# Performance work log

Hardware: AMD Instinct MI355X
Metric: run time of the kernel (lower is better)

Reference implementation:

```python
import jax, jax.numpy as jnp
import numpy as np

B, IN, H = 4096, 1024, 1024


def setup_inputs() -> dict:
    key = jax.random.key(0)
    ks = jax.random.split(key, 16)
    s_in = 1.0 / np.sqrt(IN)
    s_h = 1.0 / np.sqrt(H)
    d = {
        "x_t": jax.random.normal(ks[0], (B, IN), jnp.float32),
        "h_prev": jax.random.normal(ks[1], (B, H), jnp.float32),
        "c_prev": jax.random.normal(ks[2], (B, H), jnp.float32),
    }
    # input->hidden weights (with bias), stored torch-style as (out, in)
    for i, name in enumerate(["ii", "if", "ig", "io"]):
        d[f"W_{name}"] = jax.random.uniform(ks[3 + i], (H, IN), jnp.float32, -s_in, s_in)
        d[f"b_{name}"] = jax.random.uniform(ks[7 + i], (H,), jnp.float32, -s_in, s_in)
    # hidden->hidden weights (no bias)
    for i, name in enumerate(["hi", "hf", "hg", "ho"]):
        d[f"W_{name}"] = jax.random.uniform(ks[11 + i], (H, H), jnp.float32, -s_h, s_h)
    return d


def reference(x_t, h_prev, c_prev,
              W_ii, b_ii, W_if, b_if, W_ig, b_ig, W_io, b_io,
              W_hi, W_hf, W_hg, W_ho):
    # Fuse the 8 small GEMMs into 2 concatenated GEMMs (same math).
    Wx = jnp.concatenate([W_ii, W_if, W_ig, W_io], axis=0)   # (4H, IN)
    Wh = jnp.concatenate([W_hi, W_hf, W_hg, W_ho], axis=0)   # (4H, H)
    b = jnp.concatenate([b_ii, b_if, b_ig, b_io], axis=0)    # (4H,)
    gates = x_t @ Wx.T + h_prev @ Wh.T + b                    # (B, 4H)
    zi, zf, zg, zo = jnp.split(gates, 4, axis=1)
    i_t = jax.nn.sigmoid(zi)
    f_t = jax.nn.sigmoid(zf)
    g_t = jnp.tanh(zg)
    o_t = jax.nn.sigmoid(zo)
    c_t = f_t * c_prev + i_t * g_t
    h_t = o_t * jnp.tanh(c_t)
    return (h_t, c_t, (i_t, f_t, g_t, o_t))
```

## Files before the change

kernel.cpp:

```cpp
#include <hip/hip_runtime.h>
#include <hip/hip_bf16.h>

#define B_DIM 4096
#define K_TOT 2048
#define N_TOT 4096
#define H_DIM 1024

typedef short bf16x8 __attribute__((ext_vector_type(8)));
typedef float f32x4 __attribute__((ext_vector_type(4)));
typedef unsigned short u16x8 __attribute__((ext_vector_type(8)));

typedef __attribute__((address_space(1))) const unsigned gas_u32;
typedef __attribute__((address_space(3))) unsigned las_u32;

static __device__ __forceinline__ unsigned short f2bf(float f) {
  union { float f; unsigned u; } v; v.f = f;
  unsigned r = v.u + 0x7FFF + ((v.u >> 16) & 1);
  return (unsigned short)(r >> 16);
}

__global__ void pack_a(const float* __restrict__ x, const float* __restrict__ hp,
                       u16x8* __restrict__ A) {
  int t = blockIdx.x * blockDim.x + threadIdx.x;
  int idx = t << 3;
  int b = idx >> 11;
  int k = idx & 2047;
  const float* src = (k < 1024) ? (x + b * 1024 + k) : (hp + b * 1024 + (k - 1024));
  float4 lo = *(const float4*)src;
  float4 hi = *(const float4*)(src + 4);
  u16x8 v;
  v[0] = f2bf(lo.x); v[1] = f2bf(lo.y); v[2] = f2bf(lo.z); v[3] = f2bf(lo.w);
  v[4] = f2bf(hi.x); v[5] = f2bf(hi.y); v[6] = f2bf(hi.z); v[7] = f2bf(hi.w);
  A[t] = v;
}

__global__ void pack_w(const float* __restrict__ W0, const float* __restrict__ W1,
                       const float* __restrict__ W2, const float* __restrict__ W3,
                       const float* __restrict__ W4, const float* __restrict__ W5,
                       const float* __restrict__ W6, const float* __restrict__ W7,
                       u16x8* __restrict__ Wc) {
  int t = blockIdx.x * blockDim.x + threadIdx.x;
  int idx = t << 3;
  int n = idx >> 11;
  int k = idx & 2047;
  int gate = n >> 10;
  int j = n & 1023;
  int s = (k < 1024) ? gate : gate + 4;
  const float* base =
      (s == 0) ? W0 : (s == 1) ? W1 : (s == 2) ? W2 : (s == 3) ? W3 :
      (s == 4) ? W4 : (s == 5) ? W5 : (s == 6) ? W6 : W7;
  const float* src = base + j * 1024 + (k & 1023);
  float4 lo = *(const float4*)src;
  float4 hi = *(const float4*)(src + 4);
  u16x8 v;
  v[0] = f2bf(lo.x); v[1] = f2bf(lo.y); v[2] = f2bf(lo.z); v[3] = f2bf(lo.w);
  v[4] = f2bf(hi.x); v[5] = f2bf(hi.y); v[6] = f2bf(hi.z); v[7] = f2bf(hi.w);
  Wc[t] = v;
}

__global__ __launch_bounds__(256) void gemm_gates(
    const unsigned short* __restrict__ A,
    const unsigned short* __restrict__ W,
    float* __restrict__ G) {
  __shared__ unsigned short As[128 * 32];
  __shared__ unsigned short Bs[128 * 32];
  const int tid = threadIdx.x;
  const int wave = tid >> 6;
  const int lane = tid & 63;
  const int m0 = blockIdx.y << 7;
  const int n0 = blockIdx.x << 7;
  const int wm = (wave >> 1) << 6;
  const int wn = (wave & 1) << 6;

  f32x4 acc[4][4];
#pragma unroll
  for (int mi = 0; mi < 4; ++mi)
#pragma unroll
    for (int ni = 0; ni < 4; ++ni)
      acc[mi][ni] = (f32x4){0.f, 0.f, 0.f, 0.f};

  const int c0 = wave * 2;
  const int srow = c0 * 16 + (lane >> 2);
  const int scol = (lane & 3) * 8;
  const unsigned short* aptr0 = A + (long)(m0 + srow) * K_TOT + scol;
  const unsigned short* aptr1 = A + (long)(m0 + srow + 16) * K_TOT + scol;
  const unsigned short* bptr0 = W + (long)(n0 + srow) * K_TOT + scol;
  const unsigned short* bptr1 = W + (long)(n0 + srow + 16) * K_TOT + scol;
  char* lA0 = (char*)As + c0 * 1024;
  char* lA1 = lA0 + 1024;
  char* lB0 = (char*)Bs + c0 * 1024;
  char* lB1 = lB0 + 1024;

  const int fr = lane & 15;
  const int fko = (lane >> 4) * 16;

  for (int k0 = 0; k0 < K_TOT; k0 += 32) {
    __builtin_amdgcn_global_load_lds((gas_u32*)(aptr0 + k0), (las_u32*)lA0, 16, 0, 0);
    __builtin_amdgcn_global_load_lds((gas_u32*)(aptr1 + k0), (las_u32*)lA1, 16, 0, 0);
    __builtin_amdgcn_global_load_lds((gas_u32*)(bptr0 + k0), (las_u32*)lB0, 16, 0, 0);
    __builtin_amdgcn_global_load_lds((gas_u32*)(bptr1 + k0), (las_u32*)lB1, 16, 0, 0);
    __syncthreads();
    bf16x8 af[4], bfv[4];
#pragma unroll
    for (int i = 0; i < 4; ++i) {
      af[i]  = *(const bf16x8*)((const char*)As + (wm + i * 16 + fr) * 64 + fko);
      bfv[i] = *(const bf16x8*)((const char*)Bs + (wn + i * 16 + fr) * 64 + fko);
    }
#pragma unroll
    for (int mi = 0; mi < 4; ++mi)
#pragma unroll
      for (int ni = 0; ni < 4; ++ni)
        acc[mi][ni] = __builtin_amdgcn_mfma_f32_16x16x32_bf16(af[mi], bfv[ni], acc[mi][ni], 0, 0, 0);
    __syncthreads();
  }

  const int ccol = lane & 15;
  const int crow = (lane >> 4) * 4;
#pragma unroll
  for (int mi = 0; mi < 4; ++mi) {
#pragma unroll
    for (int ni = 0; ni < 4; ++ni) {
      float* gp = G + (long)(m0 + wm + mi * 16 + crow) * N_TOT + (n0 + wn + ni * 16 + ccol);
      gp[0]                 = acc[mi][ni][0];
      gp[N_TOT]             = acc[mi][ni][1];
      gp[2 * (long)N_TOT]   = acc[mi][ni][2];
      gp[3 * (long)N_TOT]   = acc[mi][ni][3];
    }
  }
}

static __device__ __forceinline__ float sigm(float x) {
  return 1.0f / (1.0f + __expf(-x));
}
static __device__ __forceinline__ float tanh_fast(float x) {
  x = fminf(fmaxf(x, -15.f), 15.f);
  float t = __expf(-2.0f * x);
  return (1.0f - t) / (1.0f + t);
}

__global__ void lstm_pointwise(const float* __restrict__ G, const float* __restrict__ cp,
                               const float* __restrict__ bii, const float* __restrict__ bif,
                               const float* __restrict__ big, const float* __restrict__ bio,
                               float* __restrict__ out) {
  int t = blockIdx.x * blockDim.x + threadIdx.x;
  int idx = t << 2;
  int b = idx >> 10;
  int j = idx & 1023;
  const float* gr = G + (long)b * N_TOT;
  float4 zi = *(const float4*)(gr + j);
  float4 zf = *(const float4*)(gr + 1024 + j);
  float4 zg = *(const float4*)(gr + 2048 + j);
  float4 zo = *(const float4*)(gr + 3072 + j);
  float4 vbi = *(const float4*)(bii + j);
  float4 vbf = *(const float4*)(bif + j);
  float4 vbg = *(const float4*)(big + j);
  float4 vbo = *(const float4*)(bio + j);
  float4 vc = *(const float4*)(cp + idx);

  const float* zia = (const float*)&zi; const float* zfa = (const float*)&zf;
  const float* zga = (const float*)&zg; const float* zoa = (const float*)&zo;
  const float* bia = (const float*)&vbi; const float* bfa = (const float*)&vbf;
  const float* bga = (const float*)&vbg; const float* boa = (const float*)&vbo;
  const float* vca = (const float*)&vc;

  float4 vh, vct, vi, vf, vg, vo;
  float* vha = (float*)&vh; float* vcta = (float*)&vct;
  float* via = (float*)&vi; float* vfa = (float*)&vf;
  float* vga = (float*)&vg; float* voa = (float*)&vo;
#pragma unroll
  for (int q = 0; q < 4; ++q) {
    float iv = sigm(zia[q] + bia[q]);
    float fv = sigm(zfa[q] + bfa[q]);
    float gv = tanh_fast(zga[q] + bga[q]);
    float ov = sigm(zoa[q] + boa[q]);
    float cv = fv * vca[q] + iv * gv;
    float hv = ov * tanh_fast(cv);
    via[q] = iv; vfa[q] = fv; vga[q] = gv; voa[q] = ov; vcta[q] = cv; vha[q] = hv;
  }
  const long BH = (long)B_DIM * H_DIM;
  *(float4*)(out + idx) = vh;
  *(float4*)(out + BH + idx) = vct;
  *(float4*)(out + 2 * BH + idx) = vi;
  *(float4*)(out + 3 * BH + idx) = vf;
  *(float4*)(out + 4 * BH + idx) = vg;
  *(float4*)(out + 5 * BH + idx) = vo;
}

extern "C" void kernel_launch(void* const* d_in, const int* in_sizes, int n_in,
                              void* d_out, int out_size, void* d_ws, size_t ws_size,
                              hipStream_t stream) {
  const float* x    = (const float*)d_in[0];
  const float* h    = (const float*)d_in[1];
  const float* c    = (const float*)d_in[2];
  const float* W_ii = (const float*)d_in[3];
  const float* b_ii = (const float*)d_in[4];
  const float* W_if = (const float*)d_in[5];
  const float* b_if = (const float*)d_in[6];
  const float* W_ig = (const float*)d_in[7];
  const float* b_ig = (const float*)d_in[8];
  const float* W_io = (const float*)d_in[9];
  const float* b_io = (const float*)d_in[10];
  const float* W_hi = (const float*)d_in[11];
  const float* W_hf = (const float*)d_in[12];
  const float* W_hg = (const float*)d_in[13];
  const float* W_ho = (const float*)d_in[14];

  unsigned short* Abf = (unsigned short*)d_ws;
  unsigned short* Wbf = (unsigned short*)((char*)d_ws + (size_t)16 * 1024 * 1024);
  float* G = (float*)((char*)d_ws + (size_t)32 * 1024 * 1024);

  pack_a<<<4096, 256, 0, stream>>>(x, h, (u16x8*)Abf);
  pack_w<<<4096, 256, 0, stream>>>(W_ii, W_if, W_ig, W_io, W_hi, W_hf, W_hg, W_ho,
                                   (u16x8*)Wbf);
  dim3 grid(N_TOT / 128, B_DIM / 128);
  gemm_gates<<<grid, 256, 0, stream>>>(Abf, Wbf, G);
  lstm_pointwise<<<4096, 256, 0, stream>>>(G, c, b_ii, b_if, b_ig, b_io, (float*)d_out);
}
```

Baseline: 308.8 us.

## Fuse LSTM pointwise epilogue into GEMM with gate-interleaved N tiles and LDS swizzle

Each GEMM block now gathers the matching 32 hidden columns from all four gates, so one thread holds i, f, g and o for the same element and computes the LSTM cell in the epilogue. This removes the 64MB fp32 gate buffer write and re-read and one kernel launch. It also XOR-swizzles the LDS layout of the A and B tiles to reduce bank conflicts on fragment reads. The epilogue now issues scalar stores and loads with 16-wide coalescing instead of float4 accesses, which may cost some store efficiency.

```diff
diff --git a/kernel.cpp b/kernel.cpp
--- a/kernel.cpp
+++ b/kernel.cpp
@@ -3,7 +3,6 @@
 
 #define B_DIM 4096
 #define K_TOT 2048
-#define N_TOT 4096
 #define H_DIM 1024
 
 typedef short bf16x8 __attribute__((ext_vector_type(8)));
@@ -58,19 +57,31 @@
   Wc[t] = v;
 }
 
-__global__ __launch_bounds__(256) void gemm_gates(
+static __device__ __forceinline__ float sigm(float x) {
+  return 1.0f / (1.0f + __expf(-x));
+}
+static __device__ __forceinline__ float tanh_fast(float x) {
+  x = fminf(fmaxf(x, -15.f), 15.f);
+  float t = __expf(-2.0f * x);
+  return (1.0f - t) / (1.0f + t);
+}
+
+__global__ __launch_bounds__(256) void gemm_lstm(
     const unsigned short* __restrict__ A,
     const unsigned short* __restrict__ W,
-    float* __restrict__ G) {
+    const float* __restrict__ cp,
+    const float* __restrict__ bii, const float* __restrict__ bif,
+    const float* __restrict__ big, const float* __restrict__ bio,
+    float* __restrict__ out) {
   __shared__ unsigned short As[128 * 32];
   __shared__ unsigned short Bs[128 * 32];
   const int tid = threadIdx.x;
   const int wave = tid >> 6;
   const int lane = tid & 63;
   const int m0 = blockIdx.y << 7;
-  const int n0 = blockIdx.x << 7;
+  const int j0 = blockIdx.x << 5;
   const int wm = (wave >> 1) << 6;
-  const int wn = (wave & 1) << 6;
+  const int wj16 = (wave & 1) << 4;
 
   f32x4 acc[4][4];
 #pragma unroll
@@ -80,19 +91,25 @@
       acc[mi][ni] = (f32x4){0.f, 0.f, 0.f, 0.f};
 
   const int c0 = wave * 2;
-  const int srow = c0 * 16 + (lane >> 2);
-  const int scol = (lane & 3) * 8;
-  const unsigned short* aptr0 = A + (long)(m0 + srow) * K_TOT + scol;
-  const unsigned short* aptr1 = A + (long)(m0 + srow + 16) * K_TOT + scol;
-  const unsigned short* bptr0 = W + (long)(n0 + srow) * K_TOT + scol;
-  const unsigned short* bptr1 = W + (long)(n0 + srow + 16) * K_TOT + scol;
+  const int lr = lane >> 2;
+  const int ls = lane & 3;
+  const int g  = ls ^ ((lr >> 1) & 3);
+  const unsigned short* aptr0 = A + (long)(m0 + c0 * 16 + lr) * K_TOT + g * 8;
+  const unsigned short* aptr1 = A + (long)(m0 + (c0 + 1) * 16 + lr) * K_TOT + g * 8;
+  const int rr0 = c0 * 16 + lr;
+  const int rr1 = rr0 + 16;
+  const unsigned short* bptr0 =
+      W + (long)((rr0 >> 5) * 1024 + j0 + (rr0 & 31)) * K_TOT + g * 8;
+  const unsigned short* bptr1 =
+      W + (long)((rr1 >> 5) * 1024 + j0 + (rr1 & 31)) * K_TOT + g * 8;
   char* lA0 = (char*)As + c0 * 1024;
   char* lA1 = lA0 + 1024;
   char* lB0 = (char*)Bs + c0 * 1024;
   char* lB1 = lB0 + 1024;
 
   const int fr = lane & 15;
-  const int fko = (lane >> 4) * 16;
+  const int gg = lane >> 4;
+  const int sl = (gg ^ ((fr >> 1) & 3)) * 16;
 
   for (int k0 = 0; k0 < K_TOT; k0 += 32) {
     __builtin_amdgcn_global_load_lds((gas_u32*)(aptr0 + k0), (las_u32*)lA0, 16, 0, 0);
@@ -103,8 +120,8 @@
     bf16x8 af[4], bfv[4];
 #pragma unroll
     for (int i = 0; i < 4; ++i) {
-      af[i]  = *(const bf16x8*)((const char*)As + (wm + i * 16 + fr) * 64 + fko);
-      bfv[i] = *(const bf16x8*)((const char*)Bs + (wn + i * 16 + fr) * 64 + fko);
+      af[i]  = *(const bf16x8*)((const char*)As + (wm + i * 16 + fr) * 64 + sl);
+      bfv[i] = *(const bf16x8*)((const char*)Bs + (i * 32 + wj16 + fr) * 64 + sl);
     }
 #pragma unroll
     for (int mi = 0; mi < 4; ++mi)
@@ -116,74 +133,33 @@
 
   const int ccol = lane & 15;
   const int crow = (lane >> 4) * 4;
+  const int j = j0 + wj16 + ccol;
+  const float bi = bii[j];
+  const float bff = bif[j];
+  const float bg = big[j];
+  const float bo = bio[j];
+  const long BH = (long)B_DIM * H_DIM;
 #pragma unroll
   for (int mi = 0; mi < 4; ++mi) {
 #pragma unroll
-    for (int ni = 0; ni < 4; ++ni) {
-      float* gp = G + (long)(m0 + wm + mi * 16 + crow) * N_TOT + (n0 + wn + ni * 16 + ccol);
-      gp[0]                 = acc[mi][ni][0];
-      gp[N_TOT]             = acc[mi][ni][1];
-      gp[2 * (long)N_TOT]   = acc[mi][ni][2];
-      gp[3 * (long)N_TOT]   = acc[mi][ni][3];
+    for (int reg = 0; reg < 4; ++reg) {
+      const int row = m0 + wm + mi * 16 + crow + reg;
+      const long p = (long)row * H_DIM + j;
+      const float cvp = cp[p];
+      const float iv = sigm(acc[mi][0][reg] + bi);
+      const float fv = sigm(acc[mi][1][reg] + bff);
+      const float gv = tanh_fast(acc[mi][2][reg] + bg);
+      const float ov = sigm(acc[mi][3][reg] + bo);
+      const float cv = fv * cvp + iv * gv;
+      const float hv = ov * tanh_fast(cv);
+      out[p]          = hv;
+      out[BH + p]     = cv;
+      out[2 * BH + p] = iv;
+      out[3 * BH + p] = fv;
+      out[4 * BH + p] = gv;
+      out[5 * BH + p] = ov;
     }
   }
-}
-
-static __device__ __forceinline__ float sigm(float x) {
-  return 1.0f / (1.0f + __expf(-x));
-}
-static __device__ __forceinline__ float tanh_fast(float x) {
-  x = fminf(fmaxf(x, -15.f), 15.f);
-  float t = __expf(-2.0f * x);
-  return (1.0f - t) / (1.0f + t);
-}
-
-__global__ void lstm_pointwise(const float* __restrict__ G, const float* __restrict__ cp,
-                               const float* __restrict__ bii, const float* __restrict__ bif,
-                               const float* __restrict__ big, const float* __restrict__ bio,
-                               float* __restrict__ out) {
-  int t = blockIdx.x * blockDim.x + threadIdx.x;
-  int idx = t << 2;
-  int b = idx >> 10;
-  int j = idx & 1023;
-  const float* gr = G + (long)b * N_TOT;
-  float4 zi = *(const float4*)(gr + j);
-  float4 zf = *(const float4*)(gr + 1024 + j);
-  float4 zg = *(const float4*)(gr + 2048 + j);
-  float4 zo = *(const float4*)(gr + 3072 + j);
-  float4 vbi = *(const float4*)(bii + j);
-  float4 vbf = *(const float4*)(bif + j);
-  float4 vbg = *(const float4*)(big + j);
-  float4 vbo = *(const float4*)(bio + j);
-  float4 vc = *(const float4*)(cp + idx);
-
-  const float* zia = (const float*)&zi; const float* zfa = (const float*)&zf;
-  const float* zga = (const float*)&zg; const float* zoa = (const float*)&zo;
-  const float* bia = (const float*)&vbi; const float* bfa = (const float*)&vbf;
-  const float* bga = (const float*)&vbg; const float* boa = (const float*)&vbo;
-  const float* vca = (const float*)&vc;
-
-  float4 vh, vct, vi, vf, vg, vo;
-  float* vha = (float*)&vh; float* vcta = (float*)&vct;
-  float* via = (float*)&vi; float* vfa = (float*)&vf;
-  float* vga = (float*)&vg; float* voa = (float*)&vo;
-#pragma unroll
-  for (int q = 0; q < 4; ++q) {
-    float iv = sigm(zia[q] + bia[q]);
-    float fv = sigm(zfa[q] + bfa[q]);
-    float gv = tanh_fast(zga[q] + bga[q]);
-    float ov = sigm(zoa[q] + boa[q]);
-    float cv = fv * vca[q] + iv * gv;
-    float hv = ov * tanh_fast(cv);
-    via[q] = iv; vfa[q] = fv; vga[q] = gv; voa[q] = ov; vcta[q] = cv; vha[q] = hv;
-  }
-  const long BH = (long)B_DIM * H_DIM;
-  *(float4*)(out + idx) = vh;
-  *(float4*)(out + BH + idx) = vct;
-  *(float4*)(out + 2 * BH + idx) = vi;
-  *(float4*)(out + 3 * BH + idx) = vf;
-  *(float4*)(out + 4 * BH + idx) = vg;
-  *(float4*)(out + 5 * BH + idx) = vo;
 }
 
 extern "C" void kernel_launch(void* const* d_in, const int* in_sizes, int n_in,
@@ -207,12 +183,11 @@
 
   unsigned short* Abf = (unsigned short*)d_ws;
   unsigned short* Wbf = (unsigned short*)((char*)d_ws + (size_t)16 * 1024 * 1024);
-  float* G = (float*)((char*)d_ws + (size_t)32 * 1024 * 1024);
 
   pack_a<<<4096, 256, 0, stream>>>(x, h, (u16x8*)Abf);
   pack_w<<<4096, 256, 0, stream>>>(W_ii, W_if, W_ig, W_io, W_hi, W_hf, W_hg, W_ho,
                                    (u16x8*)Wbf);
-  dim3 grid(N_TOT / 128, B_DIM / 128);
-  gemm_gates<<<grid, 256, 0, stream>>>(Abf, Wbf, G);
-  lstm_pointwise<<<4096, 256, 0, stream>>>(G, c, b_ii, b_if, b_ig, b_io, (float*)d_out);
+  dim3 grid(H_DIM / 32, B_DIM / 128);
+  gemm_lstm<<<grid, 256, 0, stream>>>(Abf, Wbf, c, b_ii, b_if, b_ig, b_io,
+                                      (float*)d_out);
 }
```

Result: faster. 282.5 us (-8.5%).
